# Performance work log

Hardware: AMD Instinct MI355X
Metric: run time of the kernel (lower is better)

## Reference

```python
import jax, jax.numpy as jnp
import numpy as np

DEGREE = 8
D = 512
K = 256
O = 512
N = 65536


def setup_inputs() -> dict:
    key = jax.random.key(0)
    ks = jax.random.split(key, 4)
    z = jax.random.normal(ks[0], (N, D), dtype=jnp.float32)
    T0 = jnp.ones((K,), dtype=jnp.float32)
    # T[i-1] corresponds to parameter T_i, i = 1..DEGREE, each [K, D]
    T = jax.random.normal(ks[1], (DEGREE, K, D), dtype=jnp.float32) * 0.02
    C_w = jax.random.normal(ks[2], (O, K), dtype=jnp.float32) * (1.0 / np.sqrt(K))
    C_b = jnp.zeros((O,), dtype=jnp.float32)
    return {"z": z, "T0": T0, "T": T, "C_w": C_w, "C_b": C_b}


def reference(z, T0, T, C_w, C_b):
    # z: [N, D]; T: [DEGREE, K, D]; recurrence over polynomial degree n:
    #   out_n = (z @ ((2n-1)/n * T_n).T) * out_{n-1} - (n-1)/n * out_{n-2}
    z = z.reshape(-1, D)
    out_prev2 = T0                                  # degree 0, [K] (broadcasts over N)
    out_prev1 = jnp.einsum('nd,kd->nk', z, T[0])    # degree 1, [N, K]
    for n in range(2, DEGREE + 1):
        a = (2.0 * n - 1.0) / n
        b = (n - 1.0) / n
        cur = jnp.einsum('nd,kd->nk', z, a * T[n - 1]) * out_prev1 - b * out_prev2
        out_prev2, out_prev1 = out_prev1, cur
    # layer_C applied to out_list[degree]
    return out_prev1 @ C_w.T + C_b
```

## Files before the change

kernel.cpp:

```cpp
#include <hip/hip_runtime.h>
#include <hip/hip_fp16.h>
#include <cstdint>

#define NROWS 65536
#define DIM   512
#define KDIM  256
#define ODIM  512
#define DEG   8
#define ZN    (NROWS * DIM)
#define TN    (DEG * KDIM * DIM)
#define CWN   (ODIM * KDIM)

typedef _Float16 f16x8 __attribute__((ext_vector_type(8)));
typedef float    f32x4 __attribute__((ext_vector_type(4)));


__device__ __forceinline__ void gld_lds16(const void* g, void* l) {
  __builtin_amdgcn_global_load_lds(
      (const __attribute__((address_space(1))) unsigned int*)g,
      (__attribute__((address_space(3))) unsigned int*)l, 16, 0, 0);
}

__device__ __forceinline__ unsigned pack2h(float a, float b) {
  union { _Float16 h[2]; unsigned u; } x;
  x.h[0] = (_Float16)a; x.h[1] = (_Float16)b;
  return x.u;
}

__device__ __forceinline__ int swz(int row, int chunk) {
  return (row << 7) | (((chunk + row) & 7) << 4);
}


__global__ void k_convert(const float* __restrict__ z,
                          const float* __restrict__ T,
                          const float* __restrict__ Cw,
                          _Float16* __restrict__ z16,
                          _Float16* __restrict__ Tb,
                          _Float16* __restrict__ Cwb) {
  long e = ((long)blockIdx.x * 256 + threadIdx.x) * 8;
  const float* src;
  _Float16* dst;
  float s = 1.0f;
  if (e < ZN) {
    src = z + e; dst = z16 + e;
  } else {
    long o = e - ZN;
    if (o < TN) {
      int n = (int)(o >> 17);
      s = (n == 0) ? 1.0f : (float)(2 * n + 1) / (float)(n + 1);
      src = T + o; dst = Tb + o;
    } else {
      long c = o - TN;
      if (c >= CWN) return;
      src = Cw + c; dst = Cwb + c;
    }
  }
  float4 v0 = *(const float4*)src;
  float4 v1 = *(const float4*)(src + 4);
  uint4 p;
  p.x = pack2h(v0.x * s, v0.y * s); p.y = pack2h(v0.z * s, v0.w * s);
  p.z = pack2h(v1.x * s, v1.y * s); p.w = pack2h(v1.z * s, v1.w * s);
  *(uint4*)dst = p;
}


__launch_bounds__(256, 2)
__global__ void k_poly(const _Float16* __restrict__ z16,
                       const float* __restrict__ T0,
                       const _Float16* __restrict__ Tb,
                       _Float16* __restrict__ u8) {
  __shared__ __align__(16) uint16_t As[256 * 64];
  __shared__ __align__(16) uint16_t Bs[128 * 64];

  const int tid = threadIdx.x;
  const int wave = tid >> 6, lane = tid & 63;

  const int id = blockIdx.x;
  const int rt = id >> 4, kg = id & 15;
  const int r0 = rt << 8;
  const int k0 = kg << 4;

  const int m_l = lane & 15, kq = lane >> 4;
  const int wrow = wave << 6;

  f32x4 acc[DEG][4];
#pragma unroll
  for (int n = 0; n < DEG; n++)
#pragma unroll
    for (int a = 0; a < 4; a++)
      acc[n][a] = (f32x4){0.f, 0.f, 0.f, 0.f};

  const _Float16* aptr[8];
  const _Float16* bptr[4];
  int lofsA[8], lofsB[4];
#pragma unroll
  for (int j = 0; j < 8; j++) {
    int lin = (j << 8) + tid;
    int row = lin >> 3;
    int c = ((lin & 7) - row) & 7;
    lofsA[j] = lin << 4;
    aptr[j] = z16 + (size_t)(r0 + row) * DIM + (c << 3);
  }
#pragma unroll
  for (int j = 0; j < 4; j++) {
    int lin = (j << 8) + tid;
    int row = lin >> 3;
    int c = ((lin & 7) - row) & 7;
    int n = row >> 4, kk = row & 15;
    lofsB[j] = lin << 4;
    bptr[j] = Tb + (size_t)((n << 8) + k0 + kk) * DIM + (c << 3);
  }

  for (int it = 0; it < DIM / 64; it++) {
    __syncthreads();
#pragma unroll
    for (int j = 0; j < 8; j++) gld_lds16(aptr[j], (char*)As + lofsA[j]);
#pragma unroll
    for (int j = 0; j < 4; j++) gld_lds16(bptr[j], (char*)Bs + lofsB[j]);
#pragma unroll
    for (int j = 0; j < 8; j++) aptr[j] += 64;
#pragma unroll
    for (int j = 0; j < 4; j++) bptr[j] += 64;
    __syncthreads();

#pragma unroll
    for (int ks = 0; ks < 2; ks++) {
      const int chunk = (ks << 2) + kq;
      f16x8 af[4];
#pragma unroll
      for (int mf = 0; mf < 4; mf++)
        af[mf] = *(const f16x8*)((char*)As + swz(wrow + (mf << 4) + m_l, chunk));
#pragma unroll
      for (int n = 0; n < DEG; n++) {
        f16x8 bv = *(const f16x8*)((char*)Bs + swz((n << 4) + m_l, chunk));
#pragma unroll
        for (int mf = 0; mf < 4; mf++)
          acc[n][mf] = __builtin_amdgcn_mfma_f32_16x16x32_f16(
              af[mf], bv, acc[n][mf], 0, 0, 0);
      }
    }
  }

  const float bcoef[7] = {1.f/2.f, 2.f/3.f, 3.f/4.f, 4.f/5.f,
                          5.f/6.f, 6.f/7.f, 7.f/8.f};
  const int col = k0 + m_l;
  const float t0v = T0[col];
#pragma unroll
  for (int mf = 0; mf < 4; mf++) {
    f32x4 up2 = {t0v, t0v, t0v, t0v};
    f32x4 up1 = acc[0][mf];
#pragma unroll
    for (int n = 2; n <= DEG; n++) {
      f32x4 cur = acc[n - 1][mf] * up1 - bcoef[n - 2] * up2;
      up2 = up1; up1 = cur;
    }
    const int rbase = r0 + wrow + (mf << 4) + (kq << 2);
#pragma unroll
    for (int r = 0; r < 4; r++)
      u8[(size_t)(rbase + r) * KDIM + col] = (_Float16)up1[r];
  }
}


__launch_bounds__(256, 3)
__global__ void k_out(const _Float16* __restrict__ u8,
                      const _Float16* __restrict__ Cwb,
                      const float* __restrict__ Cb,
                      float* __restrict__ out) {
  __shared__ __align__(16) uint16_t As[256 * 64];
  __shared__ __align__(16) uint16_t Bs[64 * 64];

  const int tid = threadIdx.x;
  const int wave = tid >> 6, lane = tid & 63;

  const int id = blockIdx.x;
  const int rt = id >> 3, cg = id & 7;
  const int r0 = rt << 8;
  const int c0 = cg << 6;

  const int m_l = lane & 15, kq = lane >> 4;
  const int wrow = wave << 6;

  f32x4 acc[4][4];
#pragma unroll
  for (int a = 0; a < 4; a++)
#pragma unroll
    for (int b = 0; b < 4; b++)
      acc[a][b] = (f32x4){0.f, 0.f, 0.f, 0.f};

  const _Float16* aptr[8];
  const _Float16* bptr[2];
  int lofsA[8], lofsB[2];
#pragma unroll
  for (int j = 0; j < 8; j++) {
    int lin = (j << 8) + tid;
    int row = lin >> 3;
    int c = ((lin & 7) - row) & 7;
    lofsA[j] = lin << 4;
    aptr[j] = u8 + (size_t)(r0 + row) * KDIM + (c << 3);
  }
#pragma unroll
  for (int j = 0; j < 2; j++) {
    int lin = (j << 8) + tid;
    int row = lin >> 3;
    int c = ((lin & 7) - row) & 7;
    lofsB[j] = lin << 4;
    bptr[j] = Cwb + (size_t)(c0 + row) * KDIM + (c << 3);
  }

  for (int it = 0; it < KDIM / 64; it++) {
    __syncthreads();
#pragma unroll
    for (int j = 0; j < 8; j++) gld_lds16(aptr[j], (char*)As + lofsA[j]);
#pragma unroll
    for (int j = 0; j < 2; j++) gld_lds16(bptr[j], (char*)Bs + lofsB[j]);
#pragma unroll
    for (int j = 0; j < 8; j++) aptr[j] += 64;
#pragma unroll
    for (int j = 0; j < 2; j++) bptr[j] += 64;
    __syncthreads();

#pragma unroll
    for (int ks = 0; ks < 2; ks++) {
      const int chunk = (ks << 2) + kq;
      f16x8 af[4];
#pragma unroll
      for (int mf = 0; mf < 4; mf++)
        af[mf] = *(const f16x8*)((char*)As + swz(wrow + (mf << 4) + m_l, chunk));
#pragma unroll
      for (int kf = 0; kf < 4; kf++) {
        f16x8 bv = *(const f16x8*)((char*)Bs + swz((kf << 4) + m_l, chunk));
#pragma unroll
        for (int mf = 0; mf < 4; mf++)
          acc[mf][kf] = __builtin_amdgcn_mfma_f32_16x16x32_f16(
              af[mf], bv, acc[mf][kf], 0, 0, 0);
      }
    }
  }

#pragma unroll
  for (int kf = 0; kf < 4; kf++) {
    const int col = c0 + (kf << 4) + m_l;
    const float cb = Cb[col];
#pragma unroll
    for (int mf = 0; mf < 4; mf++) {
      const int rbase = r0 + wrow + (mf << 4) + (kq << 2);
#pragma unroll
      for (int r = 0; r < 4; r++)
        out[(size_t)(rbase + r) * ODIM + col] = acc[mf][kf][r] + cb;
    }
  }
}


extern "C" void kernel_launch(void* const* d_in, const int* in_sizes, int n_in,
                              void* d_out, int out_size, void* d_ws, size_t ws_size,
                              hipStream_t stream) {
  const float* z  = (const float*)d_in[0];
  const float* T0 = (const float*)d_in[1];
  const float* T  = (const float*)d_in[2];
  const float* Cw = (const float*)d_in[3];
  const float* Cb = (const float*)d_in[4];
  float* out = (float*)d_out;

  char* ws = (char*)d_ws;
  _Float16* z16 = (_Float16*)ws;
  _Float16* Tb  = (_Float16*)(ws + (size_t)ZN * 2);
  _Float16* Cwb = (_Float16*)(ws + (size_t)ZN * 2 + (size_t)TN * 2);
  _Float16* u8  = (_Float16*)(ws + (size_t)ZN * 2 + (size_t)TN * 2 + (size_t)CWN * 2);

  k_convert<<<16960, 256, 0, stream>>>(z, T, Cw, z16, Tb, Cwb);
  k_poly<<<4096, 256, 0, stream>>>(z16, T0, Tb, u8);
  k_out<<<2048, 256, 0, stream>>>(u8, Cwb, Cb, out);
}
```

Baseline: 405.8 us.

## Swizzle block order for L2 reuse and stage k_out stores through LDS

Both GEMM kernels now map block IDs so that groups of 8 neighbouring row tiles share the same column/K group. The goal is more L2 reuse of the weight tiles while the z and u8 row tiles stay hot across column groups. The k_out epilogue now stages accumulators through LDS in two halves and writes the output with coalesced float4 stores and a vectorized bias add. This replaces the scattered 4-byte stores, at the cost of extra barriers and LDS traffic (possibly with bank conflicts on the scalar LDS writes).

```diff
diff --git a/kernel.cpp b/kernel.cpp
--- a/kernel.cpp
+++ b/kernel.cpp
@@ -77,7 +77,8 @@
   const int wave = tid >> 6, lane = tid & 63;
 
   const int id = blockIdx.x;
-  const int rt = id >> 4, kg = id & 15;
+  const int rt = ((id >> 7) << 3) | (id & 7);
+  const int kg = (id >> 3) & 15;
   const int r0 = rt << 8;
   const int k0 = kg << 4;
 
@@ -175,7 +176,8 @@
   const int wave = tid >> 6, lane = tid & 63;
 
   const int id = blockIdx.x;
-  const int rt = id >> 3, cg = id & 7;
+  const int rt = ((id >> 6) << 3) | (id & 7);
+  const int cg = (id >> 3) & 7;
   const int r0 = rt << 8;
   const int c0 = cg << 6;
 
@@ -239,16 +241,35 @@
     }
   }
 
-#pragma unroll
-  for (int kf = 0; kf < 4; kf++) {
-    const int col = c0 + (kf << 4) + m_l;
-    const float cb = Cb[col];
-#pragma unroll
-    for (int mf = 0; mf < 4; mf++) {
-      const int rbase = r0 + wrow + (mf << 4) + (kq << 2);
-#pragma unroll
-      for (int r = 0; r < 4; r++)
-        out[(size_t)(rbase + r) * ODIM + col] = acc[mf][kf][r] + cb;
+  float* Ts = (float*)As;
+  const int tcol = (tid & 15) << 2;
+  const int trow = tid >> 4;
+  const float4 cbv = *(const float4*)(Cb + c0 + tcol);
+#pragma unroll
+  for (int half = 0; half < 2; half++) {
+    __syncthreads();
+#pragma unroll
+    for (int mm = 0; mm < 2; mm++) {
+      const int mf = (half << 1) + mm;
+      const int cr = (wave << 5) + (mm << 4) + (kq << 2);
+#pragma unroll
+      for (int kf = 0; kf < 4; kf++) {
+        const int col = (kf << 4) + m_l;
+#pragma unroll
+        for (int r = 0; r < 4; r++)
+          Ts[(cr + r) * 64 + col] = acc[mf][kf][r];
+      }
+    }
+    __syncthreads();
+#pragma unroll
+    for (int p = 0; p < 8; p++) {
+      const int cr = (p << 4) + trow;
+      float4 v = *(const float4*)(Ts + cr * 64 + tcol);
+      const int grow = ((cr >> 5) << 6) + (half << 5) + (cr & 31);
+      float4 o;
+      o.x = v.x + cbv.x; o.y = v.y + cbv.y;
+      o.z = v.z + cbv.z; o.w = v.w + cbv.w;
+      *(float4*)(out + (size_t)(r0 + grow) * ODIM + c0 + tcol) = o;
     }
   }
 }
```

After: 393.5 us. -3.0%, faster.
